# Performance work log

Measured on AMD Instinct MI355X. Metric: run time of the kernel, lower is better.

The kernel has to match this reference:

```python
import jax, jax.numpy as jnp
import numpy as np

EPS = 1e-6

def _ln(x):
    # LayerNorm without affine, biased variance (matches torch default)
    m = jnp.mean(x, axis=-1, keepdims=True)
    v = jnp.var(x, axis=-1, keepdims=True)
    return (x - m) / jnp.sqrt(v + EPS)

def setup_inputs() -> dict:
    key = jax.random.key(0)
    ks = jax.random.split(key, 12)
    B, N, C = 8, 4096, 768
    H = C * 4
    s = 0.02
    return {
        "x":   jax.random.normal(ks[0], (B, N, C), dtype=jnp.float32),
        "Wq":  jax.random.normal(ks[1], (C, C), dtype=jnp.float32) * s,
        "bq":  jnp.zeros((C,), dtype=jnp.float32),
        "Wkv": jax.random.normal(ks[2], (C, 2 * C), dtype=jnp.float32) * s,
        "bkv": jnp.zeros((2 * C,), dtype=jnp.float32),
        "Wo":  jax.random.normal(ks[3], (C, C), dtype=jnp.float32) * s,
        "bo":  jnp.zeros((C,), dtype=jnp.float32),
        "W1":  jax.random.normal(ks[4], (C, H), dtype=jnp.float32) * s,
        "b1":  jnp.zeros((H,), dtype=jnp.float32),
        "W2":  jax.random.normal(ks[5], (H, C), dtype=jnp.float32) * s,
        "b2":  jnp.zeros((C,), dtype=jnp.float32),
    }

def reference(x, Wq, bq, Wkv, bkv, Wo, bo, W1, b1, W2, b2):
    B, N, C = x.shape
    h = 16
    d = C // h
    scale = d ** -0.5

    xn = _ln(x)                          # norm1 over full sequence
    past = xn[:, :-1, :]                 # [B, N-1, C]
    cur = xn[:, -1, :]                   # [B, C]

    q = (cur @ Wq + bq).reshape(B, h, 1, d)                 # [B,h,1,d]
    kv = past @ Wkv + bkv                                   # [B,N-1,2C]
    k, v = jnp.split(kv, 2, axis=-1)
    k = k.reshape(B, N - 1, h, d).transpose(0, 2, 1, 3)     # [B,h,N-1,d]
    v = v.reshape(B, N - 1, h, d).transpose(0, 2, 1, 3)

    sim = jnp.einsum('bhqd,bhkd->bhqk', q, k) * scale       # [B,h,1,N-1]
    attn = jax.nn.softmax(sim, axis=-1)
    out = jnp.einsum('bhqk,bhkd->bhqd', attn, v)            # [B,h,1,d]
    out = out.transpose(0, 2, 1, 3).reshape(B, C)           # [B,C]
    out = out @ Wo + bo

    last = x[:, -1, :] + out                                # attn residual
    mlp = jax.nn.gelu(_ln(last) @ W1 + b1, approximate=True) @ W2 + b2
    last = last + mlp                                       # mlp residual

    return x.at[:, -1, :].set(last)
```

## Files before the change

### kernel.cpp

```cpp
#include <hip/hip_runtime.h>

#define B_ 8
#define N_ 4096
#define C_ 768
#define NP_ 4095
#define H_ 16
#define D_ 48
#define HID_ 3072
#define SCALE 0.14433756729740643f

typedef unsigned short u16;
typedef unsigned int u32;
typedef __attribute__((ext_vector_type(4))) float f32x4;
typedef __attribute__((ext_vector_type(8))) short short8;

__device__ __forceinline__ u32 f2bf_bits(float f){
  union { float f; u32 i; } v; v.f = f;
  return (v.i + 0x7fffu + ((v.i >> 16) & 1u)) >> 16;
}
__device__ __forceinline__ u16 f2bf(float f){ return (u16)f2bf_bits(f); }
__device__ __forceinline__ float bf2f(u16 u){
  union { u32 i; float f; } v; v.i = ((u32)u) << 16; return v.f;
}
__device__ __forceinline__ u32 pack2(float a, float b){
  return f2bf_bits(a) | (f2bf_bits(b) << 16);
}

__global__ __launch_bounds__(256) void k_cs(const float* __restrict__ x,
    float* __restrict__ outp, float* __restrict__ stats)
{
  int tid = threadIdx.x;
  int l = tid & 63;
  int wid = blockIdx.x*4 + (tid>>6);
  int nw = gridDim.x*4;
  for (int row = wid; row < B_*N_; row += nw){
    const float* xr = x + (size_t)row*C_;
    float* op = outp + (size_t)row*C_;
    float4 v0 = *(const float4*)(xr + 4*l);
    float4 v1 = *(const float4*)(xr + 256 + 4*l);
    float4 v2 = *(const float4*)(xr + 512 + 4*l);
    *(float4*)(op + 4*l)       = v0;
    *(float4*)(op + 256 + 4*l) = v1;
    *(float4*)(op + 512 + 4*l) = v2;
    float s = v0.x+v0.y+v0.z+v0.w + v1.x+v1.y+v1.z+v1.w + v2.x+v2.y+v2.z+v2.w;
    float q = v0.x*v0.x+v0.y*v0.y+v0.z*v0.z+v0.w*v0.w
            + v1.x*v1.x+v1.y*v1.y+v1.z*v1.z+v1.w*v1.w
            + v2.x*v2.x+v2.y*v2.y+v2.z*v2.z+v2.w*v2.w;
    #pragma unroll
    for (int off=32; off; off>>=1){ s += __shfl_xor(s,off); q += __shfl_xor(q,off); }
    if (l==0){
      float mean = s*(1.f/C_), var = q*(1.f/C_) - mean*mean;
      ((float2*)stats)[row] = make_float2(mean, rsqrtf(var + 1e-6f));
    }
  }
}

__global__ __launch_bounds__(256) void k_q(const float* __restrict__ x,
    const float* __restrict__ Wq, const float* __restrict__ bq,
    float* __restrict__ qv, float* __restrict__ zbase)
{
  int b = blockIdx.y, t = threadIdx.x;
  int j0 = blockIdx.x*32;
  {
    int gid = (b*24 + blockIdx.x)*256 + t;
    for (int u = gid; u < 98560; u += 49152) zbase[u] = 0.f;
  }
  __shared__ float xs[C_];
  __shared__ float red[32][9];
  __shared__ float redA[4], redB[4];
  const float* xr = x + ((size_t)b*N_ + NP_)*C_;
  float v0 = xr[t], v1 = xr[t+256], v2 = xr[t+512];
  float s = v0+v1+v2, q = v0*v0+v1*v1+v2*v2;
  #pragma unroll
  for (int off=32; off; off>>=1){ s += __shfl_xor(s,off); q += __shfl_xor(q,off); }
  int w = t>>6, l = t&63;
  if (l==0){ redA[w]=s; redB[w]=q; }
  __syncthreads();
  s = redA[0]+redA[1]+redA[2]+redA[3];
  q = redB[0]+redB[1]+redB[2]+redB[3];
  float mean = s*(1.f/C_), var = q*(1.f/C_) - mean*mean;
  float rstd = rsqrtf(var + 1e-6f);
  xs[t] = (v0-mean)*rstd; xs[t+256] = (v1-mean)*rstd; xs[t+512] = (v2-mean)*rstd;
  __syncthreads();
  int jl = t&31, part = t>>5;
  const float* wp = Wq + (size_t)(part*96)*C_ + j0 + jl;
  const float* xp = xs + part*96;
  float acc = 0.f;
  #pragma unroll 8
  for (int c=0;c<96;c++) acc += xp[c]*wp[(size_t)c*C_];
  red[jl][part] = acc;
  __syncthreads();
  if (part==0){
    float a = bq[j0+jl];
    #pragma unroll
    for (int p=0;p<8;p++) a += red[jl][p];
    qv[(size_t)b*C_ + j0 + jl] = a;
  }
}

__global__ __launch_bounds__(256) void k_qw(const float* __restrict__ qv,
    const float* __restrict__ Wkv, u16* __restrict__ qWb)
{
  int b = blockIdx.y, t = threadIdx.x;
  int c0 = blockIdx.x*16;
  __shared__ float qs[C_];
  for (int u=t; u<C_; u+=256) qs[u] = qv[(size_t)b*C_+u];
  __syncthreads();
  int h = t&15, cl = t>>4;
  int c = c0 + cl;
  const float* wp = Wkv + (size_t)c*(2*C_) + h*D_;
  const float* qh = qs + h*D_;
  float acc = 0.f;
  #pragma unroll
  for (int d=0; d<D_; d++) acc += qh[d]*wp[d];
  qWb[((size_t)b*H_ + h)*C_ + c] = f2bf(acc);
}

__global__ __launch_bounds__(256) void k_sim(const float* __restrict__ x,
    const float* __restrict__ stats, const u16* __restrict__ qWb,
    u16* __restrict__ wrsT, float* __restrict__ denom, float* __restrict__ corr)
{
  int b = blockIdx.y;
  int tid = threadIdx.x;
  int w = tid>>6, l = tid&63;
  int tile = blockIdx.x*4 + w;
  int kblk = tile*16;
  int r = l&15;
  int ko = (l>>4)*8;
  float2 ms = ((const float2*)stats)[(size_t)b*N_ + kblk + r];
  float mean = ms.x, rstd = ms.y;
  const float* ar = x + ((size_t)b*N_ + kblk + r)*C_ + ko;
  const u16*  br = qWb + ((size_t)b*H_ + r)*C_ + ko;
  f32x4 acc = {0.f,0.f,0.f,0.f};
  #pragma unroll 8
  for (int s2=0;s2<24;s2++){
    float4 a0 = *(const float4*)(ar + s2*32);
    float4 a1 = *(const float4*)(ar + s2*32 + 4);
    union{uint4 u; short8 v;} A, Bf;
    A.u.x = pack2((a0.x-mean)*rstd, (a0.y-mean)*rstd);
    A.u.y = pack2((a0.z-mean)*rstd, (a0.w-mean)*rstd);
    A.u.z = pack2((a1.x-mean)*rstd, (a1.y-mean)*rstd);
    A.u.w = pack2((a1.z-mean)*rstd, (a1.w-mean)*rstd);
    Bf.u = *(const uint4*)(br + s2*32);
    acc = __builtin_amdgcn_mfma_f32_16x16x32_bf16(A.v, Bf.v, acc, 0,0,0);
  }
  int hh = l&15, mb = (l>>4)*4;
  float dsum = 0.f, csum = 0.f;
  u16* wp = wrsT + ((size_t)b*H_ + hh)*N_ + kblk + mb;
  #pragma unroll
  for (int r4=0;r4<4;r4++){
    int m = mb + r4;
    int kt = kblk + m;
    float m_mean = __shfl(mean, m);
    float m_rstd = __shfl(rstd, m);
    float wv = (kt < NP_) ? __expf(acc[r4]*SCALE) : 0.f;
    u16 wb = f2bf(wv * m_rstd);
    wp[r4] = wb;
    dsum += wv;
    csum += bf2f(wb) * m_mean;
  }
  dsum += __shfl_xor(dsum,16); csum += __shfl_xor(csum,16);
  dsum += __shfl_xor(dsum,32); csum += __shfl_xor(csum,32);
  if (l < 16){
    atomicAdd(denom + (size_t)b*H_ + l, dsum);
    atomicAdd(corr  + (size_t)b*H_ + l, csum);
  }
}

__global__ __launch_bounds__(256) void k_ctx2(const float* __restrict__ x,
    const u16* __restrict__ wrsT, float* __restrict__ ctx)
{
  int b = blockIdx.y;
  int cg = blockIdx.x % 12;
  int ks = blockIdx.x / 12;
  int tid = threadIdx.x;
  int w = tid>>6, l = tid&63;
  int ctile = cg*64 + w*16;
  int k0 = ks*512;
  const size_t xb = (size_t)b*N_*C_;
  const u16* ap = wrsT + ((size_t)b*H_ + (l&15))*N_ + k0 + (l>>4)*8;
  const float* bp = x + xb + (size_t)(k0 + (l>>4)*8)*C_ + ctile + (l&15);
  f32x4 acc = {0.f,0.f,0.f,0.f};
  for (int s=0;s<16;s++){
    union{uint4 u; short8 v;} A, Bf;
    A.u = *(const uint4*)(ap + s*32);
    const float* bq2 = bp + (size_t)s*32*C_;
    float x0 = bq2[0];
    float x1 = bq2[(size_t)1*C_];
    float x2 = bq2[(size_t)2*C_];
    float x3 = bq2[(size_t)3*C_];
    float x4 = bq2[(size_t)4*C_];
    float x5 = bq2[(size_t)5*C_];
    float x6 = bq2[(size_t)6*C_];
    float x7 = bq2[(size_t)7*C_];
    uint4 nb;
    nb.x = pack2(x0,x1); nb.y = pack2(x2,x3);
    nb.z = pack2(x4,x5); nb.w = pack2(x6,x7);
    Bf.u = nb;
    acc = __builtin_amdgcn_mfma_f32_16x16x32_bf16(A.v, Bf.v, acc, 0,0,0);
  }
  int cc = ctile + (l&15);
  float* cb = ctx + (size_t)b*H_*C_;
  #pragma unroll
  for (int r=0;r<4;r++){
    int h = (l>>4)*4 + r;
    atomicAdd(cb + h*C_ + cc, acc[r]);
  }
}

__global__ __launch_bounds__(256) void k_v(const float* __restrict__ ctx,
    const float* __restrict__ denom, const float* __restrict__ corr,
    const float* __restrict__ Wkv, const float* __restrict__ bkv,
    float* __restrict__ oat)
{
  int b = blockIdx.y, t = threadIdx.x;
  int t0 = blockIdx.x*32;
  int h0 = t0/D_;
  int h1 = (t0+31)/D_; if (h1 > H_-1) h1 = H_-1;
  __shared__ float cn[2][C_];
  __shared__ float red[32][9];
  float inv0 = 1.f/denom[(size_t)b*H_+h0];
  float inv1 = 1.f/denom[(size_t)b*H_+h1];
  float cr0 = corr[(size_t)b*H_+h0];
  float cr1 = corr[(size_t)b*H_+h1];
  for (int u=t; u<C_; u+=256){
    cn[0][u] = (ctx[((size_t)b*H_+h0)*C_+u] - cr0)*inv0;
    cn[1][u] = (ctx[((size_t)b*H_+h1)*C_+u] - cr1)*inv1;
  }
  __syncthreads();
  int jl = t&31, part = t>>5;
  int tt = t0 + jl;
  int hi = (tt/D_) - h0;
  const float* wp = Wkv + (size_t)(part*96)*(2*C_) + C_ + tt;
  const float* cp = cn[hi] + part*96;
  float acc = 0.f;
  #pragma unroll 8
  for (int c=0;c<96;c++) acc += cp[c]*wp[(size_t)c*(2*C_)];
  red[jl][part] = acc;
  __syncthreads();
  if (part==0){
    float a = bkv[C_ + tt];
    #pragma unroll
    for (int p=0;p<8;p++) a += red[jl][p];
    oat[(size_t)b*C_ + tt] = a;
  }
}

__global__ __launch_bounds__(256) void k_o(const float* __restrict__ x,
    const float* __restrict__ oat, const float* __restrict__ Wo,
    const float* __restrict__ bo, float* __restrict__ lastb)
{
  int b = blockIdx.y, t = threadIdx.x;
  int t0 = blockIdx.x*32;
  __shared__ float xs[C_];
  __shared__ float red[32][9];
  for (int u=t; u<C_; u+=256) xs[u] = oat[(size_t)b*C_+u];
  __syncthreads();
  int jl = t&31, part = t>>5;
  int tt = t0 + jl;
  const float* wp = Wo + (size_t)(part*96)*C_ + tt;
  const float* xp = xs + part*96;
  float acc = 0.f;
  #pragma unroll 8
  for (int c=0;c<96;c++) acc += xp[c]*wp[(size_t)c*C_];
  red[jl][part] = acc;
  __syncthreads();
  if (part==0){
    float a = bo[tt];
    #pragma unroll
    for (int p=0;p<8;p++) a += red[jl][p];
    lastb[(size_t)b*C_ + tt] = x[((size_t)b*N_ + NP_)*C_ + tt] + a;
  }
}

__global__ __launch_bounds__(256) void k_mlp1(const float* __restrict__ lastb,
    const float* __restrict__ W1, const float* __restrict__ b1,
    float* __restrict__ hid)
{
  int t = threadIdx.x;
  int j0 = blockIdx.x*16;
  __shared__ float xs[B_][C_];
  __shared__ float red[16][16][8];
  {
    int bb = t>>5, sub = t&31;
    const float* xr = lastb + (size_t)bb*C_;
    float s=0.f, q=0.f;
    #pragma unroll
    for (int j=0;j<24;j++){ float v = xr[sub+32*j]; s += v; q += v*v; }
    #pragma unroll
    for (int off=1; off<32; off<<=1){ s += __shfl_xor(s,off); q += __shfl_xor(q,off); }
    float mean = s*(1.f/C_), var = q*(1.f/C_) - mean*mean;
    float rstd = rsqrtf(var + 1e-6f);
    #pragma unroll
    for (int j=0;j<24;j++){ xs[bb][sub+32*j] = (xr[sub+32*j]-mean)*rstd; }
  }
  __syncthreads();
  int jl = t&15, part = t>>4;
  const float* wp = W1 + (size_t)(part*48)*HID_ + j0 + jl;
  float acc[B_];
  #pragma unroll
  for (int bb=0;bb<B_;bb++) acc[bb]=0.f;
  for (int c=0;c<48;c++){
    float wv = wp[(size_t)c*HID_];
    int cc = part*48 + c;
    #pragma unroll
    for (int bb=0;bb<B_;bb++) acc[bb] += xs[bb][cc]*wv;
  }
  #pragma unroll
  for (int bb=0;bb<B_;bb++) red[jl][part][bb] = acc[bb];
  __syncthreads();
  if (t < 128){
    int jl2 = t&15, bb = t>>4;
    float a = b1[j0+jl2];
    #pragma unroll
    for (int p=0;p<16;p++) a += red[jl2][p][bb];
    float t3 = a + 0.044715f*a*a*a;
    float g = 0.5f*a*(1.f + tanhf(0.7978845608f*t3));
    hid[(size_t)bb*HID_ + j0 + jl2] = g;
  }
}

__global__ __launch_bounds__(256) void k_mlp2(const float* __restrict__ hid,
    const float* __restrict__ W2, const float* __restrict__ b2,
    const float* __restrict__ lastb, float* __restrict__ outp)
{
  int t = threadIdx.x;
  int c0 = blockIdx.x*8;
  __shared__ float red[8][32][8];
  int ccl = t&7, part = t>>3;
  const float* wp = W2 + (size_t)(part*96)*C_ + c0 + ccl;
  float acc[B_];
  #pragma unroll
  for (int bb=0;bb<B_;bb++) acc[bb]=0.f;
  for (int j=0;j<96;j++){
    float wv = wp[(size_t)j*C_];
    int jj = part*96 + j;
    #pragma unroll
    for (int bb=0;bb<B_;bb++) acc[bb] += hid[(size_t)bb*HID_ + jj]*wv;
  }
  #pragma unroll
  for (int bb=0;bb<B_;bb++) red[ccl][part][bb] = acc[bb];
  __syncthreads();
  if (t < 64){
    int cc2 = t&7, bb = t>>3;
    float a = 0.f;
    #pragma unroll
    for (int p=0;p<32;p++) a += red[cc2][p][bb];
    int cc = c0 + cc2;
    a += b2[cc] + lastb[(size_t)bb*C_ + cc];
    outp[((size_t)bb*N_ + NP_)*C_ + cc] = a;
  }
}

extern "C" void kernel_launch(void* const* d_in, const int* in_sizes, int n_in,
                              void* d_out, int out_size, void* d_ws, size_t ws_size,
                              hipStream_t stream)
{
  (void)in_sizes; (void)n_in; (void)out_size; (void)ws_size;
  const float* x   = (const float*)d_in[0];
  const float* Wq  = (const float*)d_in[1];
  const float* bq  = (const float*)d_in[2];
  const float* Wkv = (const float*)d_in[3];
  const float* bkv = (const float*)d_in[4];
  const float* Wo  = (const float*)d_in[5];
  const float* bo  = (const float*)d_in[6];
  const float* W1  = (const float*)d_in[7];
  const float* b1  = (const float*)d_in[8];
  const float* W2  = (const float*)d_in[9];
  const float* b2  = (const float*)d_in[10];
  float* outp = (float*)d_out;
  float* ws = (float*)d_ws;
  float* ctx    = ws;
  float* denom  = ctx + 98304;
  float* corr   = denom + 128;
  float* qv     = corr + 128;
  float* oat    = qv + 6144;
  float* lastb  = oat + 6144;
  float* hid    = lastb + 6144;
  float* stats  = hid + 24576;
  u16*   qWb    = (u16*)(stats + 65536);
  u16*   wrsT   = (u16*)(stats + 65536 + 49152);

  hipLaunchKernelGGL(k_cs,   dim3(2048), dim3(256), 0, stream, x, outp, stats);
  hipLaunchKernelGGL(k_q,    dim3(24,B_), dim3(256), 0, stream, x, Wq, bq, qv, ctx);
  hipLaunchKernelGGL(k_qw,   dim3(48,B_), dim3(256), 0, stream, qv, Wkv, qWb);
  hipLaunchKernelGGL(k_sim,  dim3(64,B_), dim3(256), 0, stream, x, stats, qWb, wrsT, denom, corr);
  hipLaunchKernelGGL(k_ctx2, dim3(96,B_), dim3(256), 0, stream, x, wrsT, ctx);
  hipLaunchKernelGGL(k_v,    dim3(24,B_), dim3(256), 0, stream, ctx, denom, corr, Wkv, bkv, oat);
  hipLaunchKernelGGL(k_o,    dim3(24,B_), dim3(256), 0, stream, x, oat, Wo, bo, lastb);
  hipLaunchKernelGGL(k_mlp1, dim3(192), dim3(256), 0, stream, lastb, W1, b1, hid);
  hipLaunchKernelGGL(k_mlp2, dim3(96), dim3(256), 0, stream, hid, W2, b2, lastb, outp);
}
```

Baseline: 133.5 us.

## Fold LayerNorm stats into sim kernel, replace copy kernel with memcpy, split ctx finer

The separate row-statistics and copy kernel is removed. The full-tensor copy becomes a device-to-device memcpy, and k_sim now computes per-row mean and rstd on the fly from the raw x tiles it already loads. The normalization is applied algebraically after the MFMA, using the per-head sum of qW (computed with atomics in k_qw) as a mean correction, which avoids an extra pass over x. k_ctx2 is split into twice as many k-chunks to raise parallelism. The risk is bf16 rounding of raw rather than normalized x in the logits, plus more atomic traffic.

After: 130.4 us. 1.02x faster.

```diff
diff --git a/kernel.cpp b/kernel.cpp
--- a/kernel.cpp
+++ b/kernel.cpp
@@ -26,35 +26,6 @@
   return f2bf_bits(a) | (f2bf_bits(b) << 16);
 }
 
-__global__ __launch_bounds__(256) void k_cs(const float* __restrict__ x,
-    float* __restrict__ outp, float* __restrict__ stats)
-{
-  int tid = threadIdx.x;
-  int l = tid & 63;
-  int wid = blockIdx.x*4 + (tid>>6);
-  int nw = gridDim.x*4;
-  for (int row = wid; row < B_*N_; row += nw){
-    const float* xr = x + (size_t)row*C_;
-    float* op = outp + (size_t)row*C_;
-    float4 v0 = *(const float4*)(xr + 4*l);
-    float4 v1 = *(const float4*)(xr + 256 + 4*l);
-    float4 v2 = *(const float4*)(xr + 512 + 4*l);
-    *(float4*)(op + 4*l)       = v0;
-    *(float4*)(op + 256 + 4*l) = v1;
-    *(float4*)(op + 512 + 4*l) = v2;
-    float s = v0.x+v0.y+v0.z+v0.w + v1.x+v1.y+v1.z+v1.w + v2.x+v2.y+v2.z+v2.w;
-    float q = v0.x*v0.x+v0.y*v0.y+v0.z*v0.z+v0.w*v0.w
-            + v1.x*v1.x+v1.y*v1.y+v1.z*v1.z+v1.w*v1.w
-            + v2.x*v2.x+v2.y*v2.y+v2.z*v2.z+v2.w*v2.w;
-    #pragma unroll
-    for (int off=32; off; off>>=1){ s += __shfl_xor(s,off); q += __shfl_xor(q,off); }
-    if (l==0){
-      float mean = s*(1.f/C_), var = q*(1.f/C_) - mean*mean;
-      ((float2*)stats)[row] = make_float2(mean, rsqrtf(var + 1e-6f));
-    }
-  }
-}
-
 __global__ __launch_bounds__(256) void k_q(const float* __restrict__ x,
     const float* __restrict__ Wq, const float* __restrict__ bq,
     float* __restrict__ qv, float* __restrict__ zbase)
@@ -63,7 +34,7 @@
   int j0 = blockIdx.x*32;
   {
     int gid = (b*24 + blockIdx.x)*256 + t;
-    for (int u = gid; u < 98560; u += 49152) zbase[u] = 0.f;
+    for (int u = gid; u < 98688; u += 49152) zbase[u] = 0.f;
   }
   __shared__ float xs[C_];
   __shared__ float red[32][9];
@@ -99,11 +70,13 @@
 }
 
 __global__ __launch_bounds__(256) void k_qw(const float* __restrict__ qv,
-    const float* __restrict__ Wkv, u16* __restrict__ qWb)
+    const float* __restrict__ Wkv, u16* __restrict__ qWb,
+    float* __restrict__ qwsum)
 {
   int b = blockIdx.y, t = threadIdx.x;
   int c0 = blockIdx.x*16;
   __shared__ float qs[C_];
+  __shared__ float red2[16][17];
   for (int u=t; u<C_; u+=256) qs[u] = qv[(size_t)b*C_+u];
   __syncthreads();
   int h = t&15, cl = t>>4;
@@ -113,38 +86,53 @@
   float acc = 0.f;
   #pragma unroll
   for (int d=0; d<D_; d++) acc += qh[d]*wp[d];
-  qWb[((size_t)b*H_ + h)*C_ + c] = f2bf(acc);
+  u16 wb = f2bf(acc);
+  qWb[((size_t)b*H_ + h)*C_ + c] = wb;
+  red2[h][cl] = bf2f(wb);
+  __syncthreads();
+  if (t < 16){
+    float s2 = 0.f;
+    #pragma unroll
+    for (int j=0;j<16;j++) s2 += red2[t][j];
+    atomicAdd(qwsum + (size_t)b*H_ + t, s2);
+  }
 }
 
 __global__ __launch_bounds__(256) void k_sim(const float* __restrict__ x,
-    const float* __restrict__ stats, const u16* __restrict__ qWb,
+    const u16* __restrict__ qWb, const float* __restrict__ qwsum,
     u16* __restrict__ wrsT, float* __restrict__ denom, float* __restrict__ corr)
 {
   int b = blockIdx.y;
   int tid = threadIdx.x;
   int w = tid>>6, l = tid&63;
-  int tile = blockIdx.x*4 + w;
-  int kblk = tile*16;
+  int kblk = (blockIdx.x*4 + w)*16;
   int r = l&15;
   int ko = (l>>4)*8;
-  float2 ms = ((const float2*)stats)[(size_t)b*N_ + kblk + r];
-  float mean = ms.x, rstd = ms.y;
   const float* ar = x + ((size_t)b*N_ + kblk + r)*C_ + ko;
   const u16*  br = qWb + ((size_t)b*H_ + r)*C_ + ko;
   f32x4 acc = {0.f,0.f,0.f,0.f};
+  float s = 0.f, q = 0.f;
   #pragma unroll 8
   for (int s2=0;s2<24;s2++){
     float4 a0 = *(const float4*)(ar + s2*32);
     float4 a1 = *(const float4*)(ar + s2*32 + 4);
     union{uint4 u; short8 v;} A, Bf;
-    A.u.x = pack2((a0.x-mean)*rstd, (a0.y-mean)*rstd);
-    A.u.y = pack2((a0.z-mean)*rstd, (a0.w-mean)*rstd);
-    A.u.z = pack2((a1.x-mean)*rstd, (a1.y-mean)*rstd);
-    A.u.w = pack2((a1.z-mean)*rstd, (a1.w-mean)*rstd);
+    A.u.x = pack2(a0.x, a0.y);
+    A.u.y = pack2(a0.z, a0.w);
+    A.u.z = pack2(a1.x, a1.y);
+    A.u.w = pack2(a1.z, a1.w);
     Bf.u = *(const uint4*)(br + s2*32);
     acc = __builtin_amdgcn_mfma_f32_16x16x32_bf16(A.v, Bf.v, acc, 0,0,0);
-  }
+    s += a0.x+a0.y+a0.z+a0.w + a1.x+a1.y+a1.z+a1.w;
+    q += a0.x*a0.x+a0.y*a0.y+a0.z*a0.z+a0.w*a0.w
+       + a1.x*a1.x+a1.y*a1.y+a1.z*a1.z+a1.w*a1.w;
+  }
+  s += __shfl_xor(s,16); q += __shfl_xor(q,16);
+  s += __shfl_xor(s,32); q += __shfl_xor(q,32);
+  float mean = s*(1.f/C_), var = q*(1.f/C_) - mean*mean;
+  float rstd = rsqrtf(var + 1e-6f);
   int hh = l&15, mb = (l>>4)*4;
+  float qs = qwsum[(size_t)b*H_ + hh];
   float dsum = 0.f, csum = 0.f;
   u16* wp = wrsT + ((size_t)b*H_ + hh)*N_ + kblk + mb;
   #pragma unroll
@@ -153,7 +141,8 @@
     int kt = kblk + m;
     float m_mean = __shfl(mean, m);
     float m_rstd = __shfl(rstd, m);
-    float wv = (kt < NP_) ? __expf(acc[r4]*SCALE) : 0.f;
+    float logit = m_rstd * (acc[r4] - m_mean*qs);
+    float wv = (kt < NP_) ? __expf(logit*SCALE) : 0.f;
     u16 wb = f2bf(wv * m_rstd);
     wp[r4] = wb;
     dsum += wv;
@@ -176,12 +165,13 @@
   int tid = threadIdx.x;
   int w = tid>>6, l = tid&63;
   int ctile = cg*64 + w*16;
-  int k0 = ks*512;
+  int k0 = ks*256;
   const size_t xb = (size_t)b*N_*C_;
   const u16* ap = wrsT + ((size_t)b*H_ + (l&15))*N_ + k0 + (l>>4)*8;
   const float* bp = x + xb + (size_t)(k0 + (l>>4)*8)*C_ + ctile + (l&15);
   f32x4 acc = {0.f,0.f,0.f,0.f};
-  for (int s=0;s<16;s++){
+  #pragma unroll 4
+  for (int s=0;s<8;s++){
     union{uint4 u; short8 v;} A, Bf;
     A.u = *(const uint4*)(ap + s*32);
     const float* bq2 = bp + (size_t)s*32*C_;
@@ -373,19 +363,20 @@
   float* ctx    = ws;
   float* denom  = ctx + 98304;
   float* corr   = denom + 128;
-  float* qv     = corr + 128;
+  float* qwsum  = corr + 128;
+  float* qv     = qwsum + 128;
   float* oat    = qv + 6144;
   float* lastb  = oat + 6144;
   float* hid    = lastb + 6144;
-  float* stats  = hid + 24576;
-  u16*   qWb    = (u16*)(stats + 65536);
-  u16*   wrsT   = (u16*)(stats + 65536 + 49152);
-
-  hipLaunchKernelGGL(k_cs,   dim3(2048), dim3(256), 0, stream, x, outp, stats);
+  u16*   qWb    = (u16*)(hid + 24576);
+  u16*   wrsT   = (u16*)(hid + 24576 + 49152);
+
+  hipMemcpyAsync(outp, x, (size_t)B_*N_*C_*sizeof(float),
+                 hipMemcpyDeviceToDevice, stream);
   hipLaunchKernelGGL(k_q,    dim3(24,B_), dim3(256), 0, stream, x, Wq, bq, qv, ctx);
-  hipLaunchKernelGGL(k_qw,   dim3(48,B_), dim3(256), 0, stream, qv, Wkv, qWb);
-  hipLaunchKernelGGL(k_sim,  dim3(64,B_), dim3(256), 0, stream, x, stats, qWb, wrsT, denom, corr);
-  hipLaunchKernelGGL(k_ctx2, dim3(96,B_), dim3(256), 0, stream, x, wrsT, ctx);
+  hipLaunchKernelGGL(k_qw,   dim3(48,B_), dim3(256), 0, stream, qv, Wkv, qWb, qwsum);
+  hipLaunchKernelGGL(k_sim,  dim3(64,B_), dim3(256), 0, stream, x, qWb, qwsum, wrsT, denom, corr);
+  hipLaunchKernelGGL(k_ctx2, dim3(192,B_), dim3(256), 0, stream, x, wrsT, ctx);
   hipLaunchKernelGGL(k_v,    dim3(24,B_), dim3(256), 0, stream, ctx, denom, corr, Wkv, bkv, oat);
   hipLaunchKernelGGL(k_o,    dim3(24,B_), dim3(256), 0, stream, x, oat, Wo, bo, lastb);
   hipLaunchKernelGGL(k_mlp1, dim3(192), dim3(256), 0, stream, lastb, W1, b1, hid);
```
